# Optimization experiments

Measured on AMD Instinct MI355X. Metric: run time of the kernel, lower is better.

Reference implementation:

```python
import jax, jax.numpy as jnp
import numpy as np

N, E, F, H, L, G, EMB, C = 50000, 600000, 128, 128, 4, 64, 64, 10
BN_EPS = 1e-5


def setup_inputs() -> dict:
    key = jax.random.key(0)
    k = lambda i: jax.random.fold_in(key, i)
    s = 0.05  # weight scale
    return {
        "x": jax.random.normal(k(0), (N, F), jnp.float32),
        "edge_index": jax.random.randint(k(1), (2, E), 0, N, jnp.int64),
        "batch": jnp.sort(jax.random.randint(k(2), (N,), 0, G, jnp.int64)),
        "emb": jax.random.normal(k(3), (G, EMB), jnp.float32),
        "eps": jnp.zeros((L,), jnp.float32),
        "W1": jax.random.normal(k(4), (L, F, H), jnp.float32) * s,
        "b1": jnp.zeros((L, H), jnp.float32),
        "W2": jax.random.normal(k(5), (L, H, H), jnp.float32) * s,
        "b2": jnp.zeros((L, H), jnp.float32),
        "gamma": jnp.ones((L, H), jnp.float32),
        "beta": jnp.zeros((L, H), jnp.float32),
        "lin1_w": jax.random.normal(k(6), (L * H + EMB, 2 * H), jnp.float32) * s,
        "lin1_b": jnp.zeros((2 * H,), jnp.float32),
        "lin2_w": jax.random.normal(k(7), (2 * H, H), jnp.float32) * s,
        "lin2_b": jnp.zeros((H,), jnp.float32),
        "lin4_w": jax.random.normal(k(8), (H, C), jnp.float32) * s,
        "lin4_b": jnp.zeros((C,), jnp.float32),
    }


def _gin_mlp(h, W1, b1, W2, b2, gamma, beta):
    # Linear -> ReLU -> Linear -> ReLU -> BatchNorm1d (batch stats)
    h = jax.nn.relu(h @ W1 + b1)
    h = jax.nn.relu(h @ W2 + b2)
    mean = jnp.mean(h, axis=0)
    var = jnp.var(h, axis=0)
    return (h - mean) * jax.lax.rsqrt(var + BN_EPS) * gamma + beta


def reference(x, edge_index, batch, emb, eps, W1, b1, W2, b2, gamma, beta,
              lin1_w, lin1_b, lin2_w, lin2_b, lin4_w, lin4_b):
    src, dst = edge_index[0], edge_index[1]
    xs = []
    for l in range(L):
        # GIN: MLP((1+eps)*x_i + sum_{j->i} x_j)  via gather + scatter-add
        agg = jax.ops.segment_sum(x[src], dst, num_segments=N)  # [N,H]
        x = _gin_mlp((1.0 + eps[l]) * x + agg,
                     W1[l], b1[l], W2[l], b2[l], gamma[l], beta[l])
        xs.append(x)
    h = jnp.concatenate(xs, axis=1)  # [N, L*H]
    # global mean pool per graph
    sums = jax.ops.segment_sum(h, batch, num_segments=G)  # [G, L*H]
    cnt = jax.ops.segment_sum(jnp.ones((N,), h.dtype), batch, num_segments=G)
    pooled = sums / jnp.maximum(cnt, 1.0)[:, None]
    z = jnp.concatenate([pooled, emb.reshape(G, -1)], axis=1)
    z = jax.nn.relu(z @ lin1_w + lin1_b)  # .relu() twice is idempotent
    # dropout p=0.5 skipped (eval mode); lin3 unused in original forward
    z = jax.nn.relu(z @ lin2_w + lin2_b)
    z = z @ lin4_w + lin4_b
    return jax.nn.log_softmax(z, axis=1)
```

## Files before the change

kernel.cpp:

```cpp
#include <hip/hip_runtime.h>
#include <cstdint>
#include <cstddef>

#define N_NODES 50000
#define N_EDGES 600000
#define NLAYER  4
#define NGRAPH  64
#define SCAN_NB 196
#define NBLK_MLP ((N_NODES + 127) / 128)

typedef unsigned int   u32;
typedef unsigned short u16;
typedef unsigned char  u8;
typedef float f32x4  __attribute__((ext_vector_type(4)));
typedef short bf16x8 __attribute__((ext_vector_type(8)));
typedef u32 u32x2 __attribute__((ext_vector_type(2)));
typedef u32 u32x4 __attribute__((ext_vector_type(4)));

__device__ __forceinline__ u16 f2bf(float f) {
    u32 x = __float_as_uint(f);
    u32 r = x + 0x7fffu + ((x >> 16) & 1u);
    return (u16)(r >> 16);
}
__device__ __forceinline__ u32 pack2(float a, float b) {
    return (u32)f2bf(a) | ((u32)f2bf(b) << 16);
}

__device__ __forceinline__ u32 pk_fp8(float a, float b) {
    return (u32)__builtin_amdgcn_cvt_pk_fp8_f32(a, b, 0, false);
}
__device__ __forceinline__ float fp8b(u32 u, int j) {
    switch (j) {
    case 0:  return __builtin_amdgcn_cvt_f32_fp8(u, 0);
    case 1:  return __builtin_amdgcn_cvt_f32_fp8(u, 1);
    case 2:  return __builtin_amdgcn_cvt_f32_fp8(u, 2);
    default: return __builtin_amdgcn_cvt_f32_fp8(u, 3);
    }
}

__global__ __launch_bounds__(256) void cvt_x(const float4* __restrict__ x,
                                             u32* __restrict__ xf8) {
    int i = blockIdx.x * 256 + threadIdx.x;
    if (i < N_NODES * 32) {
        float4 v = x[i];
        u32 r = pk_fp8(v.x, v.y);
        r = (u32)__builtin_amdgcn_cvt_pk_fp8_f32(v.z, v.w, (int)r, true);
        xf8[i] = r;
    }
}

__global__ __launch_bounds__(128) void cvt_w(const float* __restrict__ W1,
                                             const float* __restrict__ W2,
                                             short* __restrict__ W1t,
                                             short* __restrict__ W2t) {
    int l = blockIdx.y, n = blockIdx.x, k = threadIdx.x;
    const float* W = blockIdx.z ? W2 : W1;
    short* Wt      = blockIdx.z ? W2t : W1t;
    Wt[((size_t)l * 128 + n) * 128 + k] = (short)f2bf(W[((size_t)l * 128 + k) * 128 + n]);
}

__global__ void count_deg(const int* __restrict__ dst, int* __restrict__ deg) {
    int e = blockIdx.x * 256 + threadIdx.x;
    if (e < N_EDGES) atomicAdd(&deg[dst[e]], 1);
}

__global__ __launch_bounds__(256) void scan_l1(const int* __restrict__ deg,
                                               int* __restrict__ bscan,
                                               int* __restrict__ bsum) {
    __shared__ int sd[256];
    int tid = threadIdx.x;
    int i = blockIdx.x * 256 + tid;
    int v = (i < N_NODES) ? deg[i] : 0;
    sd[tid] = v; __syncthreads();
#pragma unroll
    for (int off = 1; off < 256; off <<= 1) {
        int t = (tid >= off) ? sd[tid - off] : 0;
        __syncthreads();
        sd[tid] += t; __syncthreads();
    }
    if (i < N_NODES) bscan[i] = sd[tid];
    if (tid == 255) bsum[blockIdx.x] = sd[255];
}

__global__ __launch_bounds__(256) void scan_l3(const int* __restrict__ bscan,
                                               const int* __restrict__ bsum,
                                               int* __restrict__ rowp) {
    __shared__ int sd[256];
    __shared__ int sboff;
    int tid = threadIdx.x;
    int v = (tid < SCAN_NB) ? bsum[tid] : 0;
    sd[tid] = v; __syncthreads();
#pragma unroll
    for (int off = 1; off < 256; off <<= 1) {
        int t = (tid >= off) ? sd[tid - off] : 0;
        __syncthreads();
        sd[tid] += t; __syncthreads();
    }
    if (tid == (int)blockIdx.x) sboff = sd[tid] - v;
    __syncthreads();
    int i = blockIdx.x * 256 + tid;
    if (i == 0) rowp[0] = 0;
    if (i < N_NODES) rowp[i + 1] = bscan[i] + sboff;
}

__global__ void fill_csr(const int* __restrict__ src, const int* __restrict__ dst,
                         const int* __restrict__ rowp, int* __restrict__ cursor,
                         int* __restrict__ col) {
    int e = blockIdx.x * 256 + threadIdx.x;
    if (e < N_EDGES) {
        int d = dst[e];
        int pos = atomicAdd(&cursor[d], 1);
        col[rowp[d] + pos] = src[e];
    }
}

__global__ __launch_bounds__(256) void agg_kernel(
    const u8* __restrict__ xin,
    const float* __restrict__ sums,
    const float* __restrict__ gamma, const float* __restrict__ beta,
    const int* __restrict__ rowp, const int* __restrict__ col,
    const float* __restrict__ eps_all, int layer,
    u32* __restrict__ agg) {
    int node = blockIdx.x * 4 + (threadIdx.x >> 6);
    int lane = threadIdx.x & 63;
    if (node >= N_NODES) return;
    int g  = lane >> 4;
    int ch = lane & 15;

    float A[8], D[8];
    if (sums) {
        int lc = (layer - 1) * 128 + ch * 8;
#pragma unroll
        for (int j = 0; j < 8; j++) {
            int c = ch * 8 + j;
            float s1 = sums[c], s2 = sums[128 + c];
            float mean = s1 * (1.0f / N_NODES);
            float var  = s2 * (1.0f / N_NODES) - mean * mean;
            float a = rsqrtf(var + 1e-5f) * gamma[lc + j];
            A[j] = a;
            D[j] = beta[lc + j] - mean * a;
        }
    } else {
#pragma unroll
        for (int j = 0; j < 8; j++) { A[j] = 1.f; D[j] = 0.f; }
    }
    float ep = 1.0f + eps_all[layer];
    int k0 = rowp[node], k1 = rowp[node + 1];
    float s[8];
#pragma unroll
    for (int j = 0; j < 8; j++) s[j] = 0.f;

    const u8* rowbase = xin + ch * 8;
    int cc[4]; u32x2 rr[4];
    int k = k0;
    if (k < k1) {
#pragma unroll
        for (int t = 0; t < 4; t++) cc[t] = col[min(k + t * 4 + g, k1 - 1)];
#pragma unroll
        for (int t = 0; t < 4; t++) rr[t] = *(const u32x2*)(rowbase + (size_t)cc[t] * 128);
    }
    while (k < k1) {
        int kn = k + 16;
        bool more = kn < k1;
        int c2[4];
        if (more) {
#pragma unroll
            for (int t = 0; t < 4; t++) c2[t] = col[min(kn + t * 4 + g, k1 - 1)];
        }
        u32 u[8];
#pragma unroll
        for (int t = 0; t < 4; t++) {
            bool ok = (k + t * 4 + g) < k1;
            u[2 * t]     = ok ? rr[t].x : 0u;
            u[2 * t + 1] = ok ? rr[t].y : 0u;
        }
        if (more) {
#pragma unroll
            for (int t = 0; t < 4; t++) rr[t] = *(const u32x2*)(rowbase + (size_t)c2[t] * 128);
#pragma unroll
            for (int t = 0; t < 4; t++) cc[t] = c2[t];
        }
#pragma unroll
        for (int t = 0; t < 4; t++) {
#pragma unroll
            for (int j = 0; j < 4; j++) {
                s[j]     += fp8b(u[2 * t],     j);
                s[4 + j] += fp8b(u[2 * t + 1], j);
            }
        }
        k = kn;
    }
#pragma unroll
    for (int j = 0; j < 8; j++) {
        s[j] += __shfl_xor(s[j], 16);
        s[j] += __shfl_xor(s[j], 32);
    }
    u32x2 sv = *(const u32x2*)(rowbase + (size_t)node * 128);
    float deg = (float)(k1 - k0);
    float r[8];
#pragma unroll
    for (int j = 0; j < 4; j++) {
        float x0 = fp8b(sv.x, j);
        float x1 = fp8b(sv.y, j);
        r[j]     = ep * (A[j]     * x0 + D[j])     + A[j]     * s[j]     + deg * D[j];
        r[4 + j] = ep * (A[4 + j] * x1 + D[4 + j]) + A[4 + j] * s[4 + j] + deg * D[4 + j];
    }
    if (g == 0) {
        u32x4 o;
        o.x = pack2(r[0], r[1]);
        o.y = pack2(r[2], r[3]);
        o.z = pack2(r[4], r[5]);
        o.w = pack2(r[6], r[7]);
        *(u32x4*)(agg + (size_t)node * 64 + ch * 4) = o;
    }
}

#define H1_STRIDE 136
__global__ __launch_bounds__(256) void mlp_fused(
    const short* __restrict__ A,
    const short* __restrict__ W1t, const float* __restrict__ b1,
    const short* __restrict__ W2t, const float* __restrict__ b2,
    u8* __restrict__ H2, const int* __restrict__ batch,
    float* __restrict__ sums, float* __restrict__ gsum, int M) {
    __shared__ alignas(16) short h1s[128 * H1_STRIDE];
    __shared__ int sh_ga, sh_gb, sh_split;
    int tid  = threadIdx.x;
    int wave = tid >> 6, lane = tid & 63;
    int ln15 = lane & 15, quad = lane >> 4;
    int m0blk = blockIdx.x * 128;
    int m0 = m0blk + wave * 32;
    const bf16x8 zz = {0, 0, 0, 0, 0, 0, 0, 0};

    if (tid == 0) {
        int rlo = m0blk, rhi = min(m0blk + 127, M - 1);
        int ga = batch[rlo], gb = batch[rhi];
        int split = m0blk + 128;
        if (ga != gb) {
            int lo = rlo, hi = rhi;
            while (lo + 1 < hi) { int mid = (lo + hi) >> 1; if (batch[mid] == ga) lo = mid; else hi = mid; }
            split = hi;
        }
        sh_ga = ga; sh_gb = gb; sh_split = split;
    }

    bf16x8 a[2][4];
#pragma unroll
    for (int rt = 0; rt < 2; rt++) {
        int row = m0 + rt * 16 + ln15;
        const short* rp = A + (size_t)row * 128 + quad * 8;
        bool ok = row < M;
#pragma unroll
        for (int s = 0; s < 4; s++)
            a[rt][s] = ok ? *(const bf16x8*)(rp + s * 32) : zz;
    }
#pragma unroll
    for (int ct = 0; ct < 8; ct++) {
        const short* wp = W1t + (size_t)(ct * 16 + ln15) * 128 + quad * 8;
        bf16x8 b[4];
#pragma unroll
        for (int s = 0; s < 4; s++) b[s] = *(const bf16x8*)(wp + s * 32);
        float bias = b1[ct * 16 + ln15];
#pragma unroll
        for (int rt = 0; rt < 2; rt++) {
            f32x4 acc = {0.f, 0.f, 0.f, 0.f};
#pragma unroll
            for (int s = 0; s < 4; s++)
                acc = __builtin_amdgcn_mfma_f32_16x16x32_bf16(a[rt][s], b[s], acc, 0, 0, 0);
#pragma unroll
            for (int i = 0; i < 4; i++) {
                float v = fmaxf(acc[i] + bias, 0.f);
                int lr = wave * 32 + rt * 16 + quad * 4 + i;
                h1s[lr * H1_STRIDE + ct * 16 + ln15] = (short)f2bf(v);
            }
        }
    }
    __syncthreads();
    bf16x8 c[2][4];
#pragma unroll
    for (int rt = 0; rt < 2; rt++) {
        const short* rp = h1s + (size_t)(wave * 32 + rt * 16 + ln15) * H1_STRIDE + quad * 8;
#pragma unroll
        for (int s = 0; s < 4; s++) c[rt][s] = *(const bf16x8*)(rp + s * 32);
    }
    int gsplit = sh_split;
    float sAcc[8], qAcc[8], pAcc[8];
#pragma unroll
    for (int ct = 0; ct < 8; ct++) { sAcc[ct] = 0.f; qAcc[ct] = 0.f; pAcc[ct] = 0.f; }
#pragma unroll
    for (int ct = 0; ct < 8; ct++) {
        const short* wp = W2t + (size_t)(ct * 16 + ln15) * 128 + quad * 8;
        bf16x8 b[4];
#pragma unroll
        for (int s = 0; s < 4; s++) b[s] = *(const bf16x8*)(wp + s * 32);
        float bias = b2[ct * 16 + ln15];
#pragma unroll
        for (int rt = 0; rt < 2; rt++) {
            f32x4 acc = {0.f, 0.f, 0.f, 0.f};
#pragma unroll
            for (int s = 0; s < 4; s++)
                acc = __builtin_amdgcn_mfma_f32_16x16x32_bf16(c[rt][s], b[s], acc, 0, 0, 0);
            int colx = ct * 16 + ln15;
#pragma unroll
            for (int i = 0; i < 4; i++) {
                int row = m0 + rt * 16 + quad * 4 + i;
                float v = fmaxf(acc[i] + bias, 0.f);
                if (row < M) H2[(size_t)row * 128 + colx] = (u8)(pk_fp8(v, v) & 0xffu);
                float vm = (row < M) ? v : 0.f;
                sAcc[ct] += vm; qAcc[ct] += vm * vm;
                if (row < gsplit) pAcc[ct] += vm;
            }
        }
    }
    __syncthreads();
    float* scr = (float*)h1s;
    int slice = wave * 4 + quad;
#pragma unroll
    for (int ct = 0; ct < 8; ct++) {
        int colx = ct * 16 + ln15;
        scr[(0 * 16 + slice) * 128 + colx] = sAcc[ct];
        scr[(1 * 16 + slice) * 128 + colx] = qAcc[ct];
        scr[(2 * 16 + slice) * 128 + colx] = pAcc[ct];
    }
    __syncthreads();
    if (tid < 128) {
        float ss = 0.f, qq = 0.f, pa = 0.f;
#pragma unroll
        for (int sl = 0; sl < 16; sl++) {
            ss += scr[(0 * 16 + sl) * 128 + tid];
            qq += scr[(1 * 16 + sl) * 128 + tid];
            pa += scr[(2 * 16 + sl) * 128 + tid];
        }
        atomicAdd(&sums[tid], ss);
        atomicAdd(&sums[128 + tid], qq);
        int ga = sh_ga, gb = sh_gb;
        atomicAdd(&gsum[ga * 128 + tid], pa);
        if (gb != ga) atomicAdd(&gsum[gb * 128 + tid], ss - pa);
    }
}

__global__ __launch_bounds__(256) void head_kernel(
    const float* __restrict__ gsum, const float* __restrict__ sumsL,
    const float* __restrict__ gamma, const float* __restrict__ beta,
    const int* __restrict__ batch, const float* __restrict__ emb,
    const float* __restrict__ l1w, const float* __restrict__ l1b,
    const float* __restrict__ l2w, const float* __restrict__ l2b,
    const float* __restrict__ l4w, const float* __restrict__ l4b,
    float* __restrict__ out) {
    __shared__ float z[576];
    __shared__ float z1[256];
    __shared__ float z2h[2][128];
    __shared__ float z2[128];
    __shared__ float zr[128][10];
    __shared__ float inv_cnt;
    int g = blockIdx.x;
    int tid = threadIdx.x;
    if (tid == 0) {
        int lo = 0, hi = N_NODES;
        while (lo < hi) { int m = (lo + hi) >> 1; if (batch[m] < g) lo = m + 1; else hi = m; }
        int s = lo;
        lo = 0; hi = N_NODES;
        while (lo < hi) { int m = (lo + hi) >> 1; if (batch[m] < g + 1) lo = m + 1; else hi = m; }
        inv_cnt = 1.0f / fmaxf((float)(lo - s), 1.0f);
    }
    __syncthreads();
    for (int j = tid; j < 512; j += 256) {
        int l = j >> 7, c = j & 127;
        float s1 = sumsL[l * 256 + c], s2 = sumsL[l * 256 + 128 + c];
        float mean = s1 * (1.0f / N_NODES);
        float var  = s2 * (1.0f / N_NODES) - mean * mean;
        float a = rsqrtf(var + 1e-5f) * gamma[l * 128 + c];
        float d = beta[l * 128 + c] - mean * a;
        z[j] = a * gsum[(size_t)l * NGRAPH * 128 + g * 128 + c] * inv_cnt + d;
    }
    if (tid < 64) z[512 + tid] = emb[g * 64 + tid];
    __syncthreads();
    {
        float acc = l1b[tid];
        for (int j0 = 0; j0 < 576; j0 += 16) {
            float lw[16];
#pragma unroll
            for (int t = 0; t < 16; t++) lw[t] = l1w[(j0 + t) * 256 + tid];
#pragma unroll
            for (int t = 0; t < 16; t++) acc += z[j0 + t] * lw[t];
        }
        z1[tid] = fmaxf(acc, 0.f);
    }
    __syncthreads();
    {
        int c2 = tid & 127, half = tid >> 7;
        float acc = 0.f;
        int jb = half * 128;
        for (int j0 = 0; j0 < 128; j0 += 8) {
            float lw[8];
#pragma unroll
            for (int t = 0; t < 8; t++) lw[t] = l2w[(jb + j0 + t) * 128 + c2];
#pragma unroll
            for (int t = 0; t < 8; t++) acc += z1[jb + j0 + t] * lw[t];
        }
        z2h[half][c2] = acc;
    }
    __syncthreads();
    if (tid < 128) z2[tid] = fmaxf(z2h[0][tid] + z2h[1][tid] + l2b[tid], 0.f);
    __syncthreads();
    if (tid < 128) {
        float zv = z2[tid];
        const float* wr = l4w + tid * 10;
#pragma unroll
        for (int c = 0; c < 10; c++) zr[tid][c] = zv * wr[c];
    }
    __syncthreads();
    for (int s = 64; s >= 1; s >>= 1) {
        if (tid < s) {
#pragma unroll
            for (int c = 0; c < 10; c++) zr[tid][c] += zr[tid + s][c];
        }
        __syncthreads();
    }
    if (tid == 0) {
        float z3s[10];
#pragma unroll
        for (int c = 0; c < 10; c++) z3s[c] = zr[0][c] + l4b[c];
        float m = z3s[0];
        for (int i = 1; i < 10; i++) m = fmaxf(m, z3s[i]);
        float se = 0.f;
        for (int i = 0; i < 10; i++) se += expf(z3s[i] - m);
        float lse = m + logf(se);
        for (int i = 0; i < 10; i++) out[g * 10 + i] = z3s[i] - lse;
    }
}

extern "C" void kernel_launch(void* const* d_in, const int* in_sizes, int n_in,
                              void* d_out, int out_size, void* d_ws, size_t ws_size,
                              hipStream_t stream) {
    (void)in_sizes; (void)n_in; (void)out_size; (void)ws_size;
    const float* x0   = (const float*)d_in[0];
    const int* ei     = (const int*)d_in[1];
    const int* src    = ei;
    const int* dst    = ei + N_EDGES;
    const int* batch  = (const int*)d_in[2];
    const float* emb  = (const float*)d_in[3];
    const float* eps  = (const float*)d_in[4];
    const float* W1   = (const float*)d_in[5];
    const float* b1   = (const float*)d_in[6];
    const float* W2   = (const float*)d_in[7];
    const float* b2   = (const float*)d_in[8];
    const float* gamma= (const float*)d_in[9];
    const float* beta = (const float*)d_in[10];
    const float* l1w  = (const float*)d_in[11];
    const float* l1b  = (const float*)d_in[12];
    const float* l2w  = (const float*)d_in[13];
    const float* l2b  = (const float*)d_in[14];
    const float* l4w  = (const float*)d_in[15];
    const float* l4b  = (const float*)d_in[16];

    char* ws = (char*)d_ws;
    size_t off = 0;
    auto alloc = [&](size_t bytes) -> char* {
        char* p = ws + off; off += (bytes + 255) & ~(size_t)255; return p;
    };
    int* deg    = (int*)alloc(N_NODES * 4);
    int* cursor = (int*)alloc(N_NODES * 4);
    float* sumsL = (float*)alloc(NLAYER * 256 * 4);
    float* gsumL = (float*)alloc((size_t)NLAYER * NGRAPH * 128 * 4);
    size_t zero_len = (char*)gsumL - (char*)deg + (size_t)NLAYER * NGRAPH * 128 * 4;
    int* rowp   = (int*)alloc((N_NODES + 1) * 4);
    int* bscan  = (int*)alloc(N_NODES * 4);
    int* bsum   = (int*)alloc(SCAN_NB * 4);
    int* col    = (int*)alloc(N_EDGES * 4);
    u8* xf8     = (u8*)alloc((size_t)N_NODES * 128);
    u8* h2a     = (u8*)alloc((size_t)N_NODES * 128);
    u8* h2b     = (u8*)alloc((size_t)N_NODES * 128);
    u32* agg    = (u32*)alloc((size_t)N_NODES * 64 * 4);
    short* W1t  = (short*)alloc((size_t)NLAYER * 128 * 128 * 2);
    short* W2t  = (short*)alloc((size_t)NLAYER * 128 * 128 * 2);

    hipMemsetAsync(deg, 0, zero_len, stream);

    cvt_x<<<(N_NODES * 32 + 255) / 256, 256, 0, stream>>>((const float4*)x0, (u32*)xf8);
    {
        dim3 gw(128, NLAYER, 2);
        cvt_w<<<gw, 128, 0, stream>>>(W1, W2, W1t, W2t);
    }
    count_deg<<<(N_EDGES + 255) / 256, 256, 0, stream>>>(dst, deg);
    scan_l1<<<SCAN_NB, 256, 0, stream>>>(deg, bscan, bsum);
    scan_l3<<<SCAN_NB, 256, 0, stream>>>(bscan, bsum, rowp);
    fill_csr<<<(N_EDGES + 255) / 256, 256, 0, stream>>>(src, dst, rowp, cursor, col);

    const u8* xin = xf8;
    for (int l = 0; l < NLAYER; ++l) {
        u8* h2 = (l & 1) ? h2b : h2a;
        const float* sums_prev = (l == 0) ? nullptr : (sumsL + (l - 1) * 256);
        agg_kernel<<<(N_NODES + 3) / 4, 256, 0, stream>>>(
            xin, sums_prev, gamma, beta, rowp, col, eps, l, agg);
        mlp_fused<<<NBLK_MLP, 256, 0, stream>>>(
            (const short*)agg, W1t + (size_t)l * 16384, b1 + l * 128,
            W2t + (size_t)l * 16384, b2 + l * 128, h2, batch,
            sumsL + l * 256, gsumL + (size_t)l * NGRAPH * 128, N_NODES);
        xin = h2;
    }
    head_kernel<<<NGRAPH, 256, 0, stream>>>(gsumL, sumsL, gamma, beta, batch, emb,
                                            l1w, l1b, l2w, l2b, l4w, l4b,
                                            (float*)d_out);
}
```

Baseline: 446.2 us.

## Use persistent waves in aggregation and precompute BatchNorm coefficients in last MLP block

The aggregation kernel now launches a fixed grid of 2048 blocks, and each wave walks a contiguous range of about six nodes instead of handling one node per wave. This cuts block launch overhead and amortises the per-wave BatchNorm coefficient setup. The BatchNorm scale and shift are now computed once per layer by the last-finishing MLP block, found through an atomic counter, and stored to a small coefficient buffer. The agg and head kernels read that buffer instead of recomputing rsqrt from the sums in every wave. The trade-off is an extra atomic, a fence and a tail step in the MLP kernel, and possible load imbalance from the contiguous node chunks.

```diff
diff --git a/kernel.cpp b/kernel.cpp
--- a/kernel.cpp
+++ b/kernel.cpp
@@ -8,6 +8,7 @@
 #define NGRAPH  64
 #define SCAN_NB 196
 #define NBLK_MLP ((N_NODES + 127) / 128)
+#define AGG_NBLK 2048
 
 typedef unsigned int   u32;
 typedef unsigned short u16;
@@ -116,102 +117,100 @@
 
 __global__ __launch_bounds__(256) void agg_kernel(
     const u8* __restrict__ xin,
-    const float* __restrict__ sums,
-    const float* __restrict__ gamma, const float* __restrict__ beta,
+    const float* __restrict__ coef,
     const int* __restrict__ rowp, const int* __restrict__ col,
     const float* __restrict__ eps_all, int layer,
     u32* __restrict__ agg) {
-    int node = blockIdx.x * 4 + (threadIdx.x >> 6);
+    int wid  = blockIdx.x * 4 + (threadIdx.x >> 6);
     int lane = threadIdx.x & 63;
-    if (node >= N_NODES) return;
     int g  = lane >> 4;
     int ch = lane & 15;
+    const int NW  = AGG_NBLK * 4;
+    const int npw = (N_NODES + NW - 1) / NW;
+    int n0 = wid * npw;
+    if (n0 >= N_NODES) return;
+    int n1 = min(n0 + npw, N_NODES);
 
     float A[8], D[8];
-    if (sums) {
-        int lc = (layer - 1) * 128 + ch * 8;
+    if (coef) {
 #pragma unroll
         for (int j = 0; j < 8; j++) {
-            int c = ch * 8 + j;
-            float s1 = sums[c], s2 = sums[128 + c];
-            float mean = s1 * (1.0f / N_NODES);
-            float var  = s2 * (1.0f / N_NODES) - mean * mean;
-            float a = rsqrtf(var + 1e-5f) * gamma[lc + j];
-            A[j] = a;
-            D[j] = beta[lc + j] - mean * a;
+            A[j] = coef[ch * 8 + j];
+            D[j] = coef[128 + ch * 8 + j];
         }
     } else {
 #pragma unroll
         for (int j = 0; j < 8; j++) { A[j] = 1.f; D[j] = 0.f; }
     }
     float ep = 1.0f + eps_all[layer];
-    int k0 = rowp[node], k1 = rowp[node + 1];
-    float s[8];
-#pragma unroll
-    for (int j = 0; j < 8; j++) s[j] = 0.f;
-
     const u8* rowbase = xin + ch * 8;
-    int cc[4]; u32x2 rr[4];
-    int k = k0;
-    if (k < k1) {
-#pragma unroll
-        for (int t = 0; t < 4; t++) cc[t] = col[min(k + t * 4 + g, k1 - 1)];
-#pragma unroll
-        for (int t = 0; t < 4; t++) rr[t] = *(const u32x2*)(rowbase + (size_t)cc[t] * 128);
-    }
-    while (k < k1) {
-        int kn = k + 16;
-        bool more = kn < k1;
-        int c2[4];
-        if (more) {
-#pragma unroll
-            for (int t = 0; t < 4; t++) c2[t] = col[min(kn + t * 4 + g, k1 - 1)];
-        }
-        u32 u[8];
-#pragma unroll
-        for (int t = 0; t < 4; t++) {
-            bool ok = (k + t * 4 + g) < k1;
-            u[2 * t]     = ok ? rr[t].x : 0u;
-            u[2 * t + 1] = ok ? rr[t].y : 0u;
-        }
-        if (more) {
-#pragma unroll
-            for (int t = 0; t < 4; t++) rr[t] = *(const u32x2*)(rowbase + (size_t)c2[t] * 128);
-#pragma unroll
-            for (int t = 0; t < 4; t++) cc[t] = c2[t];
-        }
-#pragma unroll
-        for (int t = 0; t < 4; t++) {
-#pragma unroll
-            for (int j = 0; j < 4; j++) {
-                s[j]     += fp8b(u[2 * t],     j);
-                s[4 + j] += fp8b(u[2 * t + 1], j);
+
+    for (int node = n0; node < n1; node++) {
+        int k0 = rowp[node], k1 = rowp[node + 1];
+        float s[8];
+#pragma unroll
+        for (int j = 0; j < 8; j++) s[j] = 0.f;
+
+        int cc[4]; u32x2 rr[4];
+        int k = k0;
+        if (k < k1) {
+#pragma unroll
+            for (int t = 0; t < 4; t++) cc[t] = col[min(k + t * 4 + g, k1 - 1)];
+#pragma unroll
+            for (int t = 0; t < 4; t++) rr[t] = *(const u32x2*)(rowbase + (size_t)cc[t] * 128);
+        }
+        while (k < k1) {
+            int kn = k + 16;
+            bool more = kn < k1;
+            int c2[4];
+            if (more) {
+#pragma unroll
+                for (int t = 0; t < 4; t++) c2[t] = col[min(kn + t * 4 + g, k1 - 1)];
             }
-        }
-        k = kn;
-    }
-#pragma unroll
-    for (int j = 0; j < 8; j++) {
-        s[j] += __shfl_xor(s[j], 16);
-        s[j] += __shfl_xor(s[j], 32);
-    }
-    u32x2 sv = *(const u32x2*)(rowbase + (size_t)node * 128);
-    float deg = (float)(k1 - k0);
-    float r[8];
-#pragma unroll
-    for (int j = 0; j < 4; j++) {
-        float x0 = fp8b(sv.x, j);
-        float x1 = fp8b(sv.y, j);
-        r[j]     = ep * (A[j]     * x0 + D[j])     + A[j]     * s[j]     + deg * D[j];
-        r[4 + j] = ep * (A[4 + j] * x1 + D[4 + j]) + A[4 + j] * s[4 + j] + deg * D[4 + j];
-    }
-    if (g == 0) {
-        u32x4 o;
-        o.x = pack2(r[0], r[1]);
-        o.y = pack2(r[2], r[3]);
-        o.z = pack2(r[4], r[5]);
-        o.w = pack2(r[6], r[7]);
-        *(u32x4*)(agg + (size_t)node * 64 + ch * 4) = o;
+            u32 u[8];
+#pragma unroll
+            for (int t = 0; t < 4; t++) {
+                bool ok = (k + t * 4 + g) < k1;
+                u[2 * t]     = ok ? rr[t].x : 0u;
+                u[2 * t + 1] = ok ? rr[t].y : 0u;
+            }
+            if (more) {
+#pragma unroll
+                for (int t = 0; t < 4; t++) rr[t] = *(const u32x2*)(rowbase + (size_t)c2[t] * 128);
+            }
+#pragma unroll
+            for (int t = 0; t < 4; t++) {
+#pragma unroll
+                for (int j = 0; j < 4; j++) {
+                    s[j]     += fp8b(u[2 * t],     j);
+                    s[4 + j] += fp8b(u[2 * t + 1], j);
+                }
+            }
+            k = kn;
+        }
+#pragma unroll
+        for (int j = 0; j < 8; j++) {
+            s[j] += __shfl_xor(s[j], 16);
+            s[j] += __shfl_xor(s[j], 32);
+        }
+        u32x2 sv = *(const u32x2*)(rowbase + (size_t)node * 128);
+        float deg = (float)(k1 - k0);
+        float r[8];
+#pragma unroll
+        for (int j = 0; j < 4; j++) {
+            float x0 = fp8b(sv.x, j);
+            float x1 = fp8b(sv.y, j);
+            r[j]     = ep * (A[j]     * x0 + D[j])     + A[j]     * s[j]     + deg * D[j];
+            r[4 + j] = ep * (A[4 + j] * x1 + D[4 + j]) + A[4 + j] * s[4 + j] + deg * D[4 + j];
+        }
+        if (g == 0) {
+            u32x4 o;
+            o.x = pack2(r[0], r[1]);
+            o.y = pack2(r[2], r[3]);
+            o.z = pack2(r[4], r[5]);
+            o.w = pack2(r[6], r[7]);
+            *(u32x4*)(agg + (size_t)node * 64 + ch * 4) = o;
+        }
     }
 }
 
@@ -221,7 +220,10 @@
     const short* __restrict__ W1t, const float* __restrict__ b1,
     const short* __restrict__ W2t, const float* __restrict__ b2,
     u8* __restrict__ H2, const int* __restrict__ batch,
-    float* __restrict__ sums, float* __restrict__ gsum, int M) {
+    float* __restrict__ sums, float* __restrict__ gsum, int M,
+    int* __restrict__ red_cnt,
+    const float* __restrict__ gamma, const float* __restrict__ beta,
+    int layer, float* __restrict__ coef) {
     __shared__ alignas(16) short h1s[128 * H1_STRIDE];
     __shared__ int sh_ga, sh_gb, sh_split;
     int tid  = threadIdx.x;
@@ -336,11 +338,24 @@
         atomicAdd(&gsum[ga * 128 + tid], pa);
         if (gb != ga) atomicAdd(&gsum[gb * 128 + tid], ss - pa);
     }
+    __syncthreads();
+    __threadfence();
+    __shared__ int is_last;
+    if (tid == 0) is_last = (atomicAdd(red_cnt, 1) == (int)gridDim.x - 1) ? 1 : 0;
+    __syncthreads();
+    if (is_last && tid < 128) {
+        float s1 = atomicAdd(&sums[tid], 0.f);
+        float s2 = atomicAdd(&sums[128 + tid], 0.f);
+        float mean = s1 * (1.0f / N_NODES);
+        float var  = s2 * (1.0f / N_NODES) - mean * mean;
+        float a = rsqrtf(var + 1e-5f) * gamma[layer * 128 + tid];
+        coef[tid]       = a;
+        coef[128 + tid] = beta[layer * 128 + tid] - mean * a;
+    }
 }
 
 __global__ __launch_bounds__(256) void head_kernel(
-    const float* __restrict__ gsum, const float* __restrict__ sumsL,
-    const float* __restrict__ gamma, const float* __restrict__ beta,
+    const float* __restrict__ gsum, const float* __restrict__ coefL,
     const int* __restrict__ batch, const float* __restrict__ emb,
     const float* __restrict__ l1w, const float* __restrict__ l1b,
     const float* __restrict__ l2w, const float* __restrict__ l2b,
@@ -365,11 +380,7 @@
     __syncthreads();
     for (int j = tid; j < 512; j += 256) {
         int l = j >> 7, c = j & 127;
-        float s1 = sumsL[l * 256 + c], s2 = sumsL[l * 256 + 128 + c];
-        float mean = s1 * (1.0f / N_NODES);
-        float var  = s2 * (1.0f / N_NODES) - mean * mean;
-        float a = rsqrtf(var + 1e-5f) * gamma[l * 128 + c];
-        float d = beta[l * 128 + c] - mean * a;
+        float a = coefL[l * 256 + c], d = coefL[l * 256 + 128 + c];
         z[j] = a * gsum[(size_t)l * NGRAPH * 128 + g * 128 + c] * inv_cnt + d;
     }
     if (tid < 64) z[512 + tid] = emb[g * 64 + tid];
@@ -460,6 +471,7 @@
     };
     int* deg    = (int*)alloc(N_NODES * 4);
     int* cursor = (int*)alloc(N_NODES * 4);
+    int* red_cnt = (int*)alloc(NLAYER * 4);
     float* sumsL = (float*)alloc(NLAYER * 256 * 4);
     float* gsumL = (float*)alloc((size_t)NLAYER * NGRAPH * 128 * 4);
     size_t zero_len = (char*)gsumL - (char*)deg + (size_t)NLAYER * NGRAPH * 128 * 4;
@@ -473,6 +485,7 @@
     u32* agg    = (u32*)alloc((size_t)N_NODES * 64 * 4);
     short* W1t  = (short*)alloc((size_t)NLAYER * 128 * 128 * 2);
     short* W2t  = (short*)alloc((size_t)NLAYER * 128 * 128 * 2);
+    float* coefL = (float*)alloc(NLAYER * 256 * 4);
 
     hipMemsetAsync(deg, 0, zero_len, stream);
 
@@ -489,16 +502,17 @@
     const u8* xin = xf8;
     for (int l = 0; l < NLAYER; ++l) {
         u8* h2 = (l & 1) ? h2b : h2a;
-        const float* sums_prev = (l == 0) ? nullptr : (sumsL + (l - 1) * 256);
-        agg_kernel<<<(N_NODES + 3) / 4, 256, 0, stream>>>(
-            xin, sums_prev, gamma, beta, rowp, col, eps, l, agg);
+        const float* coef_prev = (l == 0) ? nullptr : (coefL + (l - 1) * 256);
+        agg_kernel<<<AGG_NBLK, 256, 0, stream>>>(
+            xin, coef_prev, rowp, col, eps, l, agg);
         mlp_fused<<<NBLK_MLP, 256, 0, stream>>>(
             (const short*)agg, W1t + (size_t)l * 16384, b1 + l * 128,
             W2t + (size_t)l * 16384, b2 + l * 128, h2, batch,
-            sumsL + l * 256, gsumL + (size_t)l * NGRAPH * 128, N_NODES);
+            sumsL + l * 256, gsumL + (size_t)l * NGRAPH * 128, N_NODES,
+            red_cnt + l, gamma, beta, l, coefL + l * 256);
         xin = h2;
     }
-    head_kernel<<<NGRAPH, 256, 0, stream>>>(gsumL, sumsL, gamma, beta, batch, emb,
+    head_kernel<<<NGRAPH, 256, 0, stream>>>(gsumL, coefL, batch, emb,
                                             l1w, l1b, l2w, l2b, l4w, l4b,
                                             (float*)d_out);
 }
```

New measurement: 541.0 us. 21.2% more time.
